# Optimization experiments

Hardware: AMD Instinct MI355X
Metric: run time of the kernel (lower is better)

The kernel has to match this reference:

```python
import jax, jax.numpy as jnp
import numpy as np

C = 128  # in_channels

def setup_inputs() -> dict:
    key = jax.random.key(0)
    k1, k2, k3, k4 = jax.random.split(key, 4)
    b, c, h, w = 4, C, 64, 64
    feature0 = jax.random.normal(k1, (b, c, h, w), dtype=jnp.float32)
    flow = jax.random.normal(k2, (b, 2, h, w), dtype=jnp.float32)
    # Linear weights stored torch-style as [out, in]; xavier-uniform-like scale
    lim = float(np.sqrt(6.0 / (c + c)))
    Wq = jax.random.uniform(k3, (c, c), minval=-lim, maxval=lim, dtype=jnp.float32)
    Wk = jax.random.uniform(k4, (c, c), minval=-lim, maxval=lim, dtype=jnp.float32)
    bq = jnp.zeros((c,), dtype=jnp.float32)
    bk = jnp.zeros((c,), dtype=jnp.float32)
    return {"feature0": feature0, "flow": flow, "Wq": Wq, "bq": bq, "Wk": Wk, "bk": bk}

def reference(feature0, flow, Wq, bq, Wk, bk):
    b, c, h, w = feature0.shape
    n = h * w
    # [b, n, c]
    x = feature0.reshape(b, c, n).transpose(0, 2, 1)
    query = x @ Wq.T + bq                     # q_proj(feature0)
    key = query @ Wk.T + bk                   # NOTE: k_proj applied to query (as in source)
    value = flow.reshape(b, flow.shape[1], n).transpose(0, 2, 1)  # [b, n, 2]
    scores = jnp.einsum('bnc,bmc->bnm', query, key) / jnp.sqrt(jnp.float32(c))
    prob = jax.nn.softmax(scores, axis=-1)    # [b, n, n]
    out = jnp.einsum('bnm,bmv->bnv', prob, value)  # [b, n, 2]
    return out.reshape(b, h, w, value.shape[-1]).transpose(0, 3, 1, 2)
```

## Files before the change

### kernel.cpp

```cpp
#include <hip/hip_runtime.h>
#include <hip/hip_bf16.h>

constexpr int CH = 128;
constexpr int NPOS = 4096;
constexpr int NB = 4;
constexpr int SPLITS = 8;

typedef __bf16 bf16x8 __attribute__((ext_vector_type(8)));
typedef float f32x4v __attribute__((ext_vector_type(4)));
typedef float f32x16 __attribute__((ext_vector_type(16)));

constexpr float CSC = 0.08838834764831845f * 1.4426950408889634f;


__global__ __launch_bounds__(128) void fuse_w_kernel(
    const float* __restrict__ Wq, const float* __restrict__ bq,
    const float* __restrict__ Wk, const float* __restrict__ bk,
    __bf16* __restrict__ Wqb, __bf16* __restrict__ Wqkb,
    float* __restrict__ bqk) {
  __shared__ float red[CH];
  const int o = blockIdx.x;
  const int i = threadIdx.x;
  float acc = 0.f;
#pragma unroll 8
  for (int m = 0; m < CH; m++) acc += Wk[o * CH + m] * Wq[m * CH + i];
  Wqkb[o * CH + i] = (__bf16)acc;
  Wqb[o * CH + i] = (__bf16)Wq[o * CH + i];
  red[i] = Wk[o * CH + i] * bq[i];
  __syncthreads();
  if (i == 0) {
    float s = 0.f;
    for (int m = 0; m < CH; m++) s += red[m];
    bqk[o] = s + bk[o];
  }
}

__global__ __launch_bounds__(64) void proj_kernel(
    const float* __restrict__ feature0, const __bf16* __restrict__ Wqb,
    const float* __restrict__ bq, const __bf16* __restrict__ Wqkb,
    const float* __restrict__ bqk, __bf16* __restrict__ Qf,
    __bf16* __restrict__ Kf) {
  const int lane = threadIdx.x;
  const int half = lane >> 5, l31 = lane & 31;
  const int b = blockIdx.y;
  const int pos0 = blockIdx.x * 32;
  const int pos = pos0 + l31;

  bf16x8 A[8];
#pragma unroll
  for (int ks = 0; ks < 8; ks++) {
    float v[8];
#pragma unroll
    for (int j = 0; j < 8; j++)
      v[j] = feature0[(size_t)(b * CH + ks * 16 + half * 8 + j) * NPOS + pos];
#pragma unroll
    for (int j = 0; j < 8; j++) A[ks][j] = (__bf16)v[j];
  }

#pragma unroll
  for (int z = 0; z < 2; z++) {
    const __bf16* W = z ? Wqkb : Wqb;
    const float* bias = z ? bqk : bq;
    __bf16* Out = z ? Kf : Qf;
    const float scale = z ? 1.0f : CSC;
#pragma unroll
    for (int n = 0; n < 4; n++) {
      const int co = n * 32 + l31;
      const bf16x8* Bp = (const bf16x8*)(W + co * CH + half * 8);
      f32x16 c = {0.f, 0.f, 0.f, 0.f, 0.f, 0.f, 0.f, 0.f,
                  0.f, 0.f, 0.f, 0.f, 0.f, 0.f, 0.f, 0.f};
#pragma unroll
      for (int ks = 0; ks < 8; ks++)
        c = __builtin_amdgcn_mfma_f32_32x32x16_bf16(A[ks], Bp[ks * 2], c, 0, 0,
                                                    0);
      const float bv = bias[co];
      const int quadc = l31 >> 3;
      const int j = l31 & 7;
#pragma unroll
      for (int r = 0; r < 16; r++) {
        int roff = (r & 3) + 8 * (r >> 2) + 4 * half;
        int nt = (pos0 >> 4) + (roff >> 4);
        int lp = (roff & 15) + 16 * quadc;
        Out[((((size_t)(b * (NPOS / 16) + nt)) * 4 + n) * 64 + lp) * 8 + j] =
            (__bf16)((c[r] + bv) * scale);
      }
    }
  }
}

__global__ __launch_bounds__(256, 4) void attn_kernel(
    const __bf16* __restrict__ Qf, const __bf16* __restrict__ Kf,
    const float* __restrict__ flow, float* __restrict__ part) {
  __shared__ float red[64 * 3];

  const int tid = threadIdx.x;
  const int wave = tid >> 6, lane = tid & 63;
  const int quad = lane >> 4, l15 = lane & 15;
  const int b = blockIdx.z;
  const int split = blockIdx.y;
  const int qt = blockIdx.x * 4 + wave;
  const int kbase = split * (NPOS / SPLITS);
  constexpr int NIT = NPOS / SPLITS / 32;

  const bf16x8* Qp =
      (const bf16x8*)Qf + ((size_t)(b * (NPOS / 16) + qt) * 4) * 64 + lane;
  bf16x8 qf[4];
#pragma unroll
  for (int kf = 0; kf < 4; kf++) qf[kf] = Qp[kf * 64];

  const bf16x8* Kp =
      (const bf16x8*)Kf + ((size_t)(b * (NPOS / 16) + (kbase >> 4)) * 4) * 64 +
      lane;
  const float* fl0 = flow + (size_t)(b * 2 + 0) * NPOS + kbase;
  const float* fl1 = flow + (size_t)(b * 2 + 1) * NPOS + kbase;

  float ls[4], a0[4], a1[4];
#pragma unroll
  for (int r = 0; r < 4; r++) {
    ls[r] = 0.f;
    a0[r] = 0.f;
    a1[r] = 0.f;
  }

#pragma unroll
  for (int it = 0; it < NIT; it++) {
    bf16x8 Ba[4], Bb[4];
#pragma unroll
    for (int kf = 0; kf < 4; kf++) {
      Ba[kf] = Kp[((it * 2 + 0) * 4 + kf) * 64];
      Bb[kf] = Kp[((it * 2 + 1) * 4 + kf) * 64];
    }
    const float vA0 = fl0[it * 32 + l15], vA1 = fl1[it * 32 + l15];
    const float vB0 = fl0[it * 32 + 16 + l15], vB1 = fl1[it * 32 + 16 + l15];

    f32x4v ca = {0.f, 0.f, 0.f, 0.f}, cb = {0.f, 0.f, 0.f, 0.f};
#pragma unroll
    for (int kf = 0; kf < 4; kf++)
      ca = __builtin_amdgcn_mfma_f32_16x16x32_bf16(qf[kf], Ba[kf], ca, 0, 0, 0);
#pragma unroll
    for (int kf = 0; kf < 4; kf++)
      cb = __builtin_amdgcn_mfma_f32_16x16x32_bf16(qf[kf], Bb[kf], cb, 0, 0, 0);

#pragma unroll
    for (int r = 0; r < 4; r++) {
      float pa = exp2f(ca[r]), pb = exp2f(cb[r]);
      ls[r] += pa + pb;
      a0[r] = fmaf(pa, vA0, fmaf(pb, vB0, a0[r]));
      a1[r] = fmaf(pa, vA1, fmaf(pb, vB1, a1[r]));
    }
  }

#pragma unroll
  for (int r = 0; r < 4; r++) {
#pragma unroll
    for (int st = 1; st < 16; st <<= 1) {
      ls[r] += __shfl_xor(ls[r], st, 64);
      a0[r] += __shfl_xor(a0[r], st, 64);
      a1[r] += __shfl_xor(a1[r], st, 64);
    }
  }
  if (l15 == 0) {
#pragma unroll
    for (int r = 0; r < 4; r++) {
      int ql = wave * 16 + quad * 4 + r;
      red[ql * 3 + 0] = ls[r];
      red[ql * 3 + 1] = a0[r];
      red[ql * 3 + 2] = a1[r];
    }
  }
  __syncthreads();
  for (int idx = tid; idx < 64 * 3; idx += 256) {
    int plane = idx >> 6, ql = idx & 63;
    part[((size_t)(plane * SPLITS + split) * NB + b) * NPOS + blockIdx.x * 64 +
         ql] = red[ql * 3 + plane];
  }
}

__global__ __launch_bounds__(256) void combine_kernel(
    const float* __restrict__ part, float* __restrict__ out) {
  int t = blockIdx.x * 256 + threadIdx.x;
  int b = t >> 12, q = t & (NPOS - 1);
  float l = 0.f, x = 0.f, y = 0.f;
#pragma unroll
  for (int s = 0; s < SPLITS; s++) {
    l += part[((size_t)(0 * SPLITS + s) * NB + b) * NPOS + q];
    x += part[((size_t)(1 * SPLITS + s) * NB + b) * NPOS + q];
    y += part[((size_t)(2 * SPLITS + s) * NB + b) * NPOS + q];
  }
  float inv = 1.0f / l;
  out[(size_t)(b * 2 + 0) * NPOS + q] = x * inv;
  out[(size_t)(b * 2 + 1) * NPOS + q] = y * inv;
}

extern "C" void kernel_launch(void* const* d_in, const int* in_sizes, int n_in,
                              void* d_out, int out_size, void* d_ws,
                              size_t ws_size, hipStream_t stream) {
  const float* feature0 = (const float*)d_in[0];
  const float* flow = (const float*)d_in[1];
  const float* Wq = (const float*)d_in[2];
  const float* bq = (const float*)d_in[3];
  const float* Wk = (const float*)d_in[4];
  const float* bk = (const float*)d_in[5];
  float* out = (float*)d_out;

  char* ws = (char*)d_ws;
  __bf16* Qf = (__bf16*)ws;
  __bf16* Kf = (__bf16*)(ws + (4 << 20));
  __bf16* Wqb = (__bf16*)(ws + (8 << 20));
  __bf16* Wqkb = (__bf16*)(ws + (8 << 20) + (32 << 10));
  float* bqk = (float*)(ws + (8 << 20) + (64 << 10));
  float* part = (float*)(ws + (8 << 20) + (128 << 10));

  fuse_w_kernel<<<dim3(CH), 128, 0, stream>>>(Wq, bq, Wk, bk, Wqb, Wqkb, bqk);
  proj_kernel<<<dim3(NPOS / 32, NB), 64, 0, stream>>>(feature0, Wqb, bq, Wqkb,
                                                      bqk, Qf, Kf);
  attn_kernel<<<dim3(NPOS / 64, SPLITS, NB), 256, 0, stream>>>(Qf, Kf, flow,
                                                               part);
  combine_kernel<<<dim3(NB * NPOS / 256), 256, 0, stream>>>(part, out);
}
```

Baseline: 128.6 us.

## Remap block indices for XCD-aware batch placement and double-buffer K loads

Flattens the proj and attn grids to 1-D and decodes batch and tile from the block id, so that neighbouring block ids (which are dealt out across XCDs) fall in different batches. The aim is to keep each batch's K and Q data local to a subset of XCD L2 caches. The attention inner loop also becomes a two-stage software pipeline: K fragments and flow values for the next iteration are loaded into a second register buffer while the current one is computed. This raises register pressure, which could hurt occupancy at 4 blocks per CU.

```diff
diff --git a/kernel.cpp b/kernel.cpp
--- a/kernel.cpp
+++ b/kernel.cpp
@@ -40,10 +40,12 @@
     const float* __restrict__ bq, const __bf16* __restrict__ Wqkb,
     const float* __restrict__ bqk, __bf16* __restrict__ Qf,
     __bf16* __restrict__ Kf) {
+  const int bid = blockIdx.x;
+  const int b = (bid >> 1) & 3;
+  const int u = (bid >> 3) * 2 + (bid & 1);
   const int lane = threadIdx.x;
   const int half = lane >> 5, l31 = lane & 31;
-  const int b = blockIdx.y;
-  const int pos0 = blockIdx.x * 32;
+  const int pos0 = u * 32;
   const int pos = pos0 + l31;
 
   bf16x8 A[8];
@@ -93,12 +95,16 @@
     const float* __restrict__ flow, float* __restrict__ part) {
   __shared__ float red[64 * 3];
 
+  const int bid = blockIdx.x;
+  const int b = (bid >> 1) & 3;
+  const int u = (bid >> 3) * 2 + (bid & 1);
+  const int split = u >> 6;
+  const int qg = u & 63;
+
   const int tid = threadIdx.x;
   const int wave = tid >> 6, lane = tid & 63;
   const int quad = lane >> 4, l15 = lane & 15;
-  const int b = blockIdx.z;
-  const int split = blockIdx.y;
-  const int qt = blockIdx.x * 4 + wave;
+  const int qt = qg * 4 + wave;
   const int kbase = split * (NPOS / SPLITS);
   constexpr int NIT = NPOS / SPLITS / 32;
 
@@ -122,32 +128,45 @@
     a1[r] = 0.f;
   }
 
-#pragma unroll
-  for (int it = 0; it < NIT; it++) {
-    bf16x8 Ba[4], Bb[4];
+  bf16x8 B0[8], B1[8];
+  float f0[4], f1[4];
+
+  auto load = [&](bf16x8(&B)[8], float(&fv)[4], int it) {
 #pragma unroll
     for (int kf = 0; kf < 4; kf++) {
-      Ba[kf] = Kp[((it * 2 + 0) * 4 + kf) * 64];
-      Bb[kf] = Kp[((it * 2 + 1) * 4 + kf) * 64];
-    }
-    const float vA0 = fl0[it * 32 + l15], vA1 = fl1[it * 32 + l15];
-    const float vB0 = fl0[it * 32 + 16 + l15], vB1 = fl1[it * 32 + 16 + l15];
-
+      B[kf] = Kp[((it * 2 + 0) * 4 + kf) * 64];
+      B[4 + kf] = Kp[((it * 2 + 1) * 4 + kf) * 64];
+    }
+    fv[0] = fl0[it * 32 + l15];
+    fv[1] = fl1[it * 32 + l15];
+    fv[2] = fl0[it * 32 + 16 + l15];
+    fv[3] = fl1[it * 32 + 16 + l15];
+  };
+  auto compute = [&](const bf16x8(&B)[8], const float(&fv)[4]) {
     f32x4v ca = {0.f, 0.f, 0.f, 0.f}, cb = {0.f, 0.f, 0.f, 0.f};
 #pragma unroll
     for (int kf = 0; kf < 4; kf++)
-      ca = __builtin_amdgcn_mfma_f32_16x16x32_bf16(qf[kf], Ba[kf], ca, 0, 0, 0);
+      ca = __builtin_amdgcn_mfma_f32_16x16x32_bf16(qf[kf], B[kf], ca, 0, 0, 0);
 #pragma unroll
     for (int kf = 0; kf < 4; kf++)
-      cb = __builtin_amdgcn_mfma_f32_16x16x32_bf16(qf[kf], Bb[kf], cb, 0, 0, 0);
-
+      cb = __builtin_amdgcn_mfma_f32_16x16x32_bf16(qf[kf], B[4 + kf], cb, 0, 0,
+                                                   0);
 #pragma unroll
     for (int r = 0; r < 4; r++) {
       float pa = exp2f(ca[r]), pb = exp2f(cb[r]);
       ls[r] += pa + pb;
-      a0[r] = fmaf(pa, vA0, fmaf(pb, vB0, a0[r]));
-      a1[r] = fmaf(pa, vA1, fmaf(pb, vB1, a1[r]));
-    }
+      a0[r] = fmaf(pa, fv[0], fmaf(pb, fv[2], a0[r]));
+      a1[r] = fmaf(pa, fv[1], fmaf(pb, fv[3], a1[r]));
+    }
+  };
+
+  load(B0, f0, 0);
+#pragma unroll
+  for (int it = 0; it < NIT; it += 2) {
+    if (it + 1 < NIT) load(B1, f1, it + 1);
+    compute(B0, f0);
+    if (it + 2 < NIT) load(B0, f0, it + 2);
+    if (it + 1 < NIT) compute(B1, f1);
   }
 
 #pragma unroll
@@ -171,8 +190,8 @@
   __syncthreads();
   for (int idx = tid; idx < 64 * 3; idx += 256) {
     int plane = idx >> 6, ql = idx & 63;
-    part[((size_t)(plane * SPLITS + split) * NB + b) * NPOS + blockIdx.x * 64 +
-         ql] = red[ql * 3 + plane];
+    part[((size_t)(plane * SPLITS + split) * NB + b) * NPOS + qg * 64 + ql] =
+        red[ql * 3 + plane];
   }
 }
 
@@ -212,9 +231,8 @@
   float* part = (float*)(ws + (8 << 20) + (128 << 10));
 
   fuse_w_kernel<<<dim3(CH), 128, 0, stream>>>(Wq, bq, Wk, bk, Wqb, Wqkb, bqk);
-  proj_kernel<<<dim3(NPOS / 32, NB), 64, 0, stream>>>(feature0, Wqb, bq, Wqkb,
-                                                      bqk, Qf, Kf);
-  attn_kernel<<<dim3(NPOS / 64, SPLITS, NB), 256, 0, stream>>>(Qf, Kf, flow,
-                                                               part);
+  proj_kernel<<<dim3(512), 64, 0, stream>>>(feature0, Wqb, bq, Wqkb, bqk, Qf,
+                                            Kf);
+  attn_kernel<<<dim3(2048), 256, 0, stream>>>(Qf, Kf, flow, part);
   combine_kernel<<<dim3(NB * NPOS / 256), 256, 0, stream>>>(part, out);
 }
```

After: 131.7 us. 1.02x slower.
